# Kernel tuning notes

Hardware: AMD Instinct MI355X
Metric: run time of the kernel (lower is better)

## Reference

```python
import jax, jax.numpy as jnp
import numpy as np
from jax import lax

DN = ('NHWC', 'HWIO', 'NHWC')


def _conv(x, w):
    # x: [B,H,W,Cin], w: [kh,kw,Cin,Cout], 'same' padding
    return lax.conv_general_dilated(x, w, (1, 1), 'SAME', dimension_numbers=DN)


def _hard_sigmoid(x):
    # Keras hard_sigmoid: clip(0.2*x + 0.5, 0, 1)
    return jnp.clip(0.2 * x + 0.5, 0.0, 1.0)


def convlstm2d(x, Wk, Uk, b, filters):
    """Keras ConvLSTM2D, return_sequences=True, padding='same'.
    x: [B,T,H,W,Cin]. Gate order in kernel: [i, f, c, o].
    Returns h sequence [B,T,H,W,filters].
    """
    B, T, H, W, _ = x.shape
    h0 = jnp.zeros((B, H, W, filters), x.dtype)
    c0 = jnp.zeros((B, H, W, filters), x.dtype)

    def step(carry, xt):
        h, c = carry
        z = _conv(xt, Wk) + _conv(h, Uk) + b  # [B,H,W,4*filters]
        zi, zf, zc, zo = jnp.split(z, 4, axis=-1)
        i = _hard_sigmoid(zi)
        f = _hard_sigmoid(zf)
        o = _hard_sigmoid(zo)
        c_new = f * c + i * jnp.tanh(zc)
        h_new = o * jnp.tanh(c_new)
        return (h_new, c_new), h_new

    xs = jnp.moveaxis(x, 1, 0)  # [T,B,H,W,Cin]
    _, hs = lax.scan(step, (h0, c0), xs)
    return jnp.moveaxis(hs, 0, 1)  # [B,T,H,W,filters]


def setup_inputs() -> dict:
    key = jax.random.key(0)
    ks = jax.random.split(key, 7)
    B, T, H, W, Cin, F = 8, 10, 64, 64, 32, 64
    s = 0.05
    return {
        'x': jax.random.normal(ks[0], (B, T, H, W, Cin), jnp.float32),
        'Wk1': jax.random.normal(ks[1], (5, 5, Cin, 4 * F), jnp.float32) * s,
        'Uk1': jax.random.normal(ks[2], (5, 5, F, 4 * F), jnp.float32) * s,
        'b1': jnp.zeros((4 * F,), jnp.float32),
        'Wk2': jax.random.normal(ks[3], (3, 3, F, 4 * F), jnp.float32) * s,
        'Uk2': jax.random.normal(ks[4], (3, 3, F, 4 * F), jnp.float32) * s,
        'b2': jnp.zeros((4 * F,), jnp.float32),
    }


def reference(x, Wk1, Uk1, b1, Wk2, Uk2, b2):
    F = Uk1.shape[2]
    y = jax.nn.relu(convlstm2d(x, Wk1, Uk1, b1, F))
    y = jax.nn.relu(convlstm2d(y, Wk2, Uk2, b2, F))
    return y
```

## Files before the change

kernel.cpp:

```cpp
#include <hip/hip_runtime.h>
#include <cstdint>
#include <cmath>


#define NT 256

typedef __attribute__((ext_vector_type(8))) short short8;
typedef __attribute__((ext_vector_type(4))) float f32x4;

__device__ __forceinline__ float hsig(float v) {
    return fminf(fmaxf(fmaf(v, 0.2f, 0.5f), 0.0f), 1.0f);
}

__device__ __forceinline__ short bf16rnd(float f) {
    union { float f; unsigned u; } a; a.f = f;
    return (short)((a.u + 0x7FFFu + ((a.u >> 16) & 1u)) >> 16);
}

__device__ __forceinline__ void split_bf16(float f, short& h, short& l) {
    h = bf16rnd(f);
    union { unsigned u; float f; } b; b.u = ((unsigned)(unsigned short)h) << 16;
    l = bf16rnd(f - b.f);
}

__device__ __forceinline__ float from_bf16(short s) {
    union { unsigned u; float f; } b; b.u = ((unsigned)(unsigned short)s) << 16;
    return b.f;
}

template<int CIN, int KS>
__device__ __forceinline__ void conv_mfma(
    const short* __restrict__ P,
    const short* __restrict__ Bpk,
    f32x4 (&acc)[4][4],
    short* lds,
    int y, int fg, int lane, int tid)
{
    constexpr int PAD   = KS / 2;
    constexpr int COLS  = 64 + 2 * PAD;
    constexpr int PST   = 2 * CIN + 8;
    constexpr int CH    = CIN / 32;
    constexpr int VPP   = (2 * CIN) / 8;
    constexpr int NLOAD = COLS * VPP;
    constexpr int NV    = (NLOAD + NT - 1) / NT;

    uint4 vals[NV];

    auto load_row = [&](int ky) {
        int yin = y + ky - PAD;
        const short* rowp = P + (size_t)yin * 64 * 2 * CIN;
        #pragma unroll
        for (int i = 0; i < NV; ++i) {
            int idx = tid + i * NT;
            uint4 z; z.x = 0; z.y = 0; z.z = 0; z.w = 0;
            if (idx < NLOAD) {
                int col = idx / VPP;
                int v   = idx - col * VPP;
                int g   = col - PAD;
                if (yin >= 0 && yin < 64 && g >= 0 && g < 64)
                    z = *(const uint4*)(rowp + (size_t)g * 2 * CIN + v * 8);
            }
            vals[i] = z;
        }
    };

    load_row(0);
    for (int ky = 0; ky < KS; ++ky) {
        __syncthreads();
        #pragma unroll
        for (int i = 0; i < NV; ++i) {
            int idx = tid + i * NT;
            if (idx < NLOAD) {
                int col = idx / VPP;
                int v   = idx - col * VPP;
                *(uint4*)(lds + col * PST + v * 8) = vals[i];
            }
        }
        __syncthreads();
        if (ky + 1 < KS) load_row(ky + 1);

        int yin = y + ky - PAD;
        if (yin >= 0 && yin < 64) {
            for (int kx = 0; kx < KS; ++kx) {
                int tap = ky * KS + kx;
                #pragma unroll
                for (int ch = 0; ch < CH; ++ch) {
                    int choff = ch * 32 + ((lane >> 4) & 3) * 8;
                    short8 ah[4], al[4];
                    #pragma unroll
                    for (int mt = 0; mt < 4; ++mt) {
                        int col = mt * 16 + (lane & 15) + kx;
                        const short* base = lds + col * PST + choff;
                        ah[mt] = *(const short8*)base;
                        al[mt] = *(const short8*)(base + CIN);
                    }
                    const short* bp = Bpk
                        + ((size_t)((tap * CH + ch) * 16 + fg)) * 1024
                        + lane * 16;
                    #pragma unroll
                    for (int g = 0; g < 4; ++g) {
                        short8 bh = *(const short8*)bp;
                        short8 bl = *(const short8*)(bp + 8);
                        bp += 4096;
                        #pragma unroll
                        for (int mt = 0; mt < 4; ++mt) {
                            acc[g][mt] = __builtin_amdgcn_mfma_f32_16x16x32_bf16(
                                ah[mt], bh, acc[g][mt], 0, 0, 0);
                            acc[g][mt] = __builtin_amdgcn_mfma_f32_16x16x32_bf16(
                                al[mt], bh, acc[g][mt], 0, 0, 0);
                            acc[g][mt] = __builtin_amdgcn_mfma_f32_16x16x32_bf16(
                                ah[mt], bl, acc[g][mt], 0, 0, 0);
                        }
                    }
                }
            }
        }
    }
}

template<int CIN_X, int KS, bool WRITE_SEQ>
__global__ __launch_bounds__(NT, 2)
void convlstm_step(
    const short* __restrict__ xp, long xp_bstride,
    const short* __restrict__ h_prev,
    float* __restrict__ c_state,
    const short* __restrict__ Wpk,
    const short* __restrict__ Upk,
    const float* __restrict__ bias,
    short* __restrict__ h_next,
    short* __restrict__ seq, long seq_bstride)
{
    __shared__ __align__(16) short lds[9248];

    const int tid  = threadIdx.x;
    const int lane = tid & 63;
    const int fg   = tid >> 6;
    const int q    = (lane >> 4) & 3;
    const int batch = blockIdx.x >> 6;
    const int y     = blockIdx.x & 63;

    f32x4 acc[4][4];
    #pragma unroll
    for (int g = 0; g < 4; ++g)
        #pragma unroll
        for (int mt = 0; mt < 4; ++mt)
            #pragma unroll
            for (int r = 0; r < 4; ++r) acc[g][mt][r] = 0.0f;

    conv_mfma<CIN_X, KS>(xp + (size_t)batch * xp_bstride, Wpk, acc, lds, y, fg, lane, tid);
    conv_mfma<64,    KS>(h_prev + (size_t)batch * 4096 * 128, Upk, acc, lds, y, fg, lane, tid);

    const int fl = fg * 16 + (lane & 15);
    const float b_i = bias[fl];
    const float b_f = bias[64 + fl];
    const float b_c = bias[128 + fl];
    const float b_o = bias[192 + fl];

    const long pixbase = (long)batch * 4096 + (long)y * 64;
    const long cb = pixbase * 64 + fl;
    const long sb = (long)batch * seq_bstride + ((long)y * 64) * 128 + fl;

    #pragma unroll
    for (int mt = 0; mt < 4; ++mt) {
        #pragma unroll
        for (int r = 0; r < 4; ++r) {
            int col = mt * 16 + q * 4 + r;
            long cidx = cb + (long)col * 64;
            float zi = acc[0][mt][r] + b_i;
            float zf = acc[1][mt][r] + b_f;
            float zc = acc[2][mt][r] + b_c;
            float zo = acc[3][mt][r] + b_o;
            float ig = hsig(zi);
            float fgt = hsig(zf);
            float og = hsig(zo);
            float cp = c_state[cidx];
            float cn = fgt * cp + ig * tanhf(zc);
            float hn = og * tanhf(cn);
            c_state[cidx] = cn;

            short hh, hl;
            split_bf16(hn, hh, hl);
            long hoff = (pixbase + col) * 128 + fl;
            h_next[hoff]      = hh;
            h_next[hoff + 64] = hl;
            if (WRITE_SEQ) {
                bool pos = hn > 0.0f;
                seq[sb + (long)col * 128]      = pos ? hh : (short)0;
                seq[sb + (long)col * 128 + 64] = pos ? hl : (short)0;
            }
        }
    }
}

__global__ void convert_planes32(const float4* __restrict__ src,
                                 unsigned* __restrict__ dst, int n4)
{
    int t = blockIdx.x * NT + threadIdx.x;
    if (t >= n4) return;
    int pix = t >> 3;
    int c4  = t & 7;
    float4 v = src[t];
    short h0, l0, h1, l1, h2, l2, h3, l3;
    split_bf16(v.x, h0, l0);
    split_bf16(v.y, h1, l1);
    split_bf16(v.z, h2, l2);
    split_bf16(v.w, h3, l3);
    unsigned* p = dst + (size_t)pix * 32;
    p[c4 * 2]      = (unsigned)(unsigned short)h0 | ((unsigned)(unsigned short)h1 << 16);
    p[c4 * 2 + 1]  = (unsigned)(unsigned short)h2 | ((unsigned)(unsigned short)h3 << 16);
    p[16 + c4 * 2]     = (unsigned)(unsigned short)l0 | ((unsigned)(unsigned short)l1 << 16);
    p[16 + c4 * 2 + 1] = (unsigned)(unsigned short)l2 | ((unsigned)(unsigned short)l3 << 16);
}

__global__ void repack(const float* __restrict__ src, short* __restrict__ dst,
                       int KS, int CH)
{
    int total = KS * KS * CH * 16 * 64;
    int t = blockIdx.x * NT + threadIdx.x;
    if (t >= total) return;
    int u = t >> 6, lane = t & 63;
    int tap = u / (CH * 16);
    int rem = u - tap * (CH * 16);
    int ch = rem >> 4;
    int gfg = rem & 15;
    int g = gfg >> 2, fgp = gfg & 3;
    int CIN = CH * 32;
    int n = lane & 15, qq = lane >> 4;
    short* d = dst + (size_t)u * 1024 + lane * 16;
    int gc = g * 64 + fgp * 16 + n;
    for (int j = 0; j < 8; ++j) {
        int c = ch * 32 + qq * 8 + j;
        float w = src[((size_t)tap * CIN + c) * 256 + gc];
        short h, l;
        split_bf16(w, h, l);
        d[j] = h;
        d[8 + j] = l;
    }
}

__global__ void relu_copy(const short* __restrict__ hp, float* __restrict__ out,
                          long out_bstride)
{
    long i = (long)blockIdx.x * NT + threadIdx.x;
    long pix = i >> 6;
    int c = (int)(i & 63);
    float f = from_bf16(hp[pix * 128 + c]) + from_bf16(hp[pix * 128 + 64 + c]);
    long b = pix >> 12;
    long within = (pix & 4095) * 64 + c;
    out[b * out_bstride + within] = fmaxf(f, 0.0f);
}

extern "C" void kernel_launch(void* const* d_in, const int* in_sizes, int n_in,
                              void* d_out, int out_size, void* d_ws, size_t ws_size,
                              hipStream_t stream) {
    const float* x   = (const float*)d_in[0];
    const float* Wk1 = (const float*)d_in[1];
    const float* Uk1 = (const float*)d_in[2];
    const float* b1  = (const float*)d_in[3];
    const float* Wk2 = (const float*)d_in[4];
    const float* Uk2 = (const float*)d_in[5];
    const float* b2  = (const float*)d_in[6];
    float* out = (float*)d_out;

    const long S  = (long)8 * 64 * 64 * 64;
    const long oT = (long)64 * 64 * 64;
    const long oB = 10 * oT;

    short* h_a = (short*)d_ws;
    short* h_b = h_a + 2 * S;
    float* c_s = (float*)(h_b + 2 * S);
    short* Wp1 = (short*)(c_s + S);
    short* Up1 = Wp1 + 25 * 1 * 16 * 1024;
    short* Wp2 = Up1 + 25 * 2 * 16 * 1024;
    short* Up2 = Wp2 + 9 * 2 * 16 * 1024;
    short* x1p = Up2 + 9 * 2 * 16 * 1024;
    const long x1pN = (long)8 * 10 * 4096 * 64;
    (void)x1pN; (void)ws_size;

    {
        int n4 = 8 * 10 * 4096 * 8;
        convert_planes32<<<dim3((n4 + NT - 1) / NT), dim3(NT), 0, stream>>>(
            (const float4*)x, (unsigned*)x1p, n4);
    }
    repack<<<dim3((25 * 1 * 16 * 64 + NT - 1) / NT), dim3(NT), 0, stream>>>(Wk1, Wp1, 5, 1);
    repack<<<dim3((25 * 2 * 16 * 64 + NT - 1) / NT), dim3(NT), 0, stream>>>(Uk1, Up1, 5, 2);
    repack<<<dim3((9 * 2 * 16 * 64 + NT - 1) / NT), dim3(NT), 0, stream>>>(Wk2, Wp2, 3, 2);
    repack<<<dim3((9 * 2 * 16 * 64 + NT - 1) / NT), dim3(NT), 0, stream>>>(Uk2, Up2, 3, 2);

    short* seqs = (short*)d_out;

    hipMemsetAsync(h_a, 0, (size_t)S * 4, stream);
    hipMemsetAsync(c_s, 0, (size_t)S * 4, stream);
    short* hc = h_a;
    short* hn = h_b;
    const long x1T = (long)4096 * 64;
    const long x1B = 10 * x1T;
    for (int t = 0; t < 10; ++t) {
        convlstm_step<32, 5, true><<<dim3(512), dim3(NT), 0, stream>>>(
            x1p + t * x1T, x1B, hc, c_s, Wp1, Up1, b1, hn,
            seqs + t * oT * 2, oB * 2);
        short* tmp = hc; hc = hn; hn = tmp;
    }

    hipMemsetAsync(hc, 0, (size_t)S * 4, stream);
    hipMemsetAsync(c_s, 0, (size_t)S * 4, stream);
    for (int t = 0; t < 10; ++t) {
        convlstm_step<64, 3, false><<<dim3(512), dim3(NT), 0, stream>>>(
            seqs + t * oT * 2, oB * 2, hc, c_s, Wp2, Up2, b2, hn,
            nullptr, 0);
        relu_copy<<<dim3(8192), dim3(NT), 0, stream>>>(hn, out + t * oT, oB);
        short* tmp = hc; hc = hn; hn = tmp;
    }
}
```

Baseline: 1.946 ms.

## Split rows across two 2-wave blocks, fuse x/h convs, prefetch weights in registers

The step kernel now uses 128-thread blocks, each covering half of the filter groups for one output row, which doubles the grid to 1024 blocks. The x and h convolutions are merged into a single loop over kernel rows that stages both input rows in separate LDS buffers. Padding is handled by zero-filling LDS once and skipping out-of-range kernel rows. Weight fragments for the next tap/segment are software-prefetched into registers so global loads overlap the MFMAs. This costs more register pressure and duplicates the input-row loads across the two half-blocks.

```diff
diff --git a/kernel.cpp b/kernel.cpp
--- a/kernel.cpp
+++ b/kernel.cpp
@@ -3,7 +3,8 @@
 #include <cmath>
 
 
-#define NT 256
+#define NT  128
+#define NTU 256
 
 typedef __attribute__((ext_vector_type(8))) short short8;
 typedef __attribute__((ext_vector_type(4))) float f32x4;
@@ -28,97 +29,9 @@
     return b.f;
 }
 
-template<int CIN, int KS>
-__device__ __forceinline__ void conv_mfma(
-    const short* __restrict__ P,
-    const short* __restrict__ Bpk,
-    f32x4 (&acc)[4][4],
-    short* lds,
-    int y, int fg, int lane, int tid)
-{
-    constexpr int PAD   = KS / 2;
-    constexpr int COLS  = 64 + 2 * PAD;
-    constexpr int PST   = 2 * CIN + 8;
-    constexpr int CH    = CIN / 32;
-    constexpr int VPP   = (2 * CIN) / 8;
-    constexpr int NLOAD = COLS * VPP;
-    constexpr int NV    = (NLOAD + NT - 1) / NT;
-
-    uint4 vals[NV];
-
-    auto load_row = [&](int ky) {
-        int yin = y + ky - PAD;
-        const short* rowp = P + (size_t)yin * 64 * 2 * CIN;
-        #pragma unroll
-        for (int i = 0; i < NV; ++i) {
-            int idx = tid + i * NT;
-            uint4 z; z.x = 0; z.y = 0; z.z = 0; z.w = 0;
-            if (idx < NLOAD) {
-                int col = idx / VPP;
-                int v   = idx - col * VPP;
-                int g   = col - PAD;
-                if (yin >= 0 && yin < 64 && g >= 0 && g < 64)
-                    z = *(const uint4*)(rowp + (size_t)g * 2 * CIN + v * 8);
-            }
-            vals[i] = z;
-        }
-    };
-
-    load_row(0);
-    for (int ky = 0; ky < KS; ++ky) {
-        __syncthreads();
-        #pragma unroll
-        for (int i = 0; i < NV; ++i) {
-            int idx = tid + i * NT;
-            if (idx < NLOAD) {
-                int col = idx / VPP;
-                int v   = idx - col * VPP;
-                *(uint4*)(lds + col * PST + v * 8) = vals[i];
-            }
-        }
-        __syncthreads();
-        if (ky + 1 < KS) load_row(ky + 1);
-
-        int yin = y + ky - PAD;
-        if (yin >= 0 && yin < 64) {
-            for (int kx = 0; kx < KS; ++kx) {
-                int tap = ky * KS + kx;
-                #pragma unroll
-                for (int ch = 0; ch < CH; ++ch) {
-                    int choff = ch * 32 + ((lane >> 4) & 3) * 8;
-                    short8 ah[4], al[4];
-                    #pragma unroll
-                    for (int mt = 0; mt < 4; ++mt) {
-                        int col = mt * 16 + (lane & 15) + kx;
-                        const short* base = lds + col * PST + choff;
-                        ah[mt] = *(const short8*)base;
-                        al[mt] = *(const short8*)(base + CIN);
-                    }
-                    const short* bp = Bpk
-                        + ((size_t)((tap * CH + ch) * 16 + fg)) * 1024
-                        + lane * 16;
-                    #pragma unroll
-                    for (int g = 0; g < 4; ++g) {
-                        short8 bh = *(const short8*)bp;
-                        short8 bl = *(const short8*)(bp + 8);
-                        bp += 4096;
-                        #pragma unroll
-                        for (int mt = 0; mt < 4; ++mt) {
-                            acc[g][mt] = __builtin_amdgcn_mfma_f32_16x16x32_bf16(
-                                ah[mt], bh, acc[g][mt], 0, 0, 0);
-                            acc[g][mt] = __builtin_amdgcn_mfma_f32_16x16x32_bf16(
-                                al[mt], bh, acc[g][mt], 0, 0, 0);
-                            acc[g][mt] = __builtin_amdgcn_mfma_f32_16x16x32_bf16(
-                                ah[mt], bl, acc[g][mt], 0, 0, 0);
-                        }
-                    }
-                }
-            }
-        }
-    }
-}
-
-template<int CIN_X, int KS, bool WRITE_SEQ>
+struct BF { uint4 bh[4]; uint4 bl[4]; };
+
+template<int CINX, int KS, bool WRITE_SEQ>
 __global__ __launch_bounds__(NT, 2)
 void convlstm_step(
     const short* __restrict__ xp, long xp_bstride,
@@ -130,14 +43,39 @@
     short* __restrict__ h_next,
     short* __restrict__ seq, long seq_bstride)
 {
-    __shared__ __align__(16) short lds[9248];
+    constexpr int PAD  = KS / 2;
+    constexpr int COLS = 64 + 2 * PAD;
+    constexpr int CHX  = CINX / 32;
+    constexpr int SEGS = CHX + 2;
+    constexpr int PSTX = 2 * CINX + 8;
+    constexpr int PSTH = 136;
+    constexpr int VPPX = CINX / 4;
+
+    __shared__ __align__(16) short xs[COLS * PSTX];
+    __shared__ __align__(16) short hs[COLS * PSTH];
 
     const int tid  = threadIdx.x;
     const int lane = tid & 63;
-    const int fg   = tid >> 6;
-    const int q    = (lane >> 4) & 3;
-    const int batch = blockIdx.x >> 6;
-    const int y     = blockIdx.x & 63;
+    const int wid  = tid >> 6;
+    const int q8   = ((lane >> 4) & 3) * 8;
+    const int bi   = blockIdx.x;
+    const int batch = bi >> 7;
+    const int rem   = bi & 127;
+    const int y     = rem >> 1;
+    const int half  = rem & 1;
+    const int fg    = half * 2 + wid;
+
+    const short* xim = xp + (size_t)batch * xp_bstride;
+    const short* him = h_prev + (size_t)batch * 4096 * 128;
+
+    for (int idx = tid; idx < (COLS * PSTX) / 8; idx += NT) {
+        uint4 z; z.x = 0; z.y = 0; z.z = 0; z.w = 0;
+        *(uint4*)(xs + idx * 8) = z;
+    }
+    for (int idx = tid; idx < (COLS * PSTH) / 8; idx += NT) {
+        uint4 z; z.x = 0; z.y = 0; z.z = 0; z.w = 0;
+        *(uint4*)(hs + idx * 8) = z;
+    }
 
     f32x4 acc[4][4];
     #pragma unroll
@@ -147,14 +85,92 @@
             #pragma unroll
             for (int r = 0; r < 4; ++r) acc[g][mt][r] = 0.0f;
 
-    conv_mfma<CIN_X, KS>(xp + (size_t)batch * xp_bstride, Wpk, acc, lds, y, fg, lane, tid);
-    conv_mfma<64,    KS>(h_prev + (size_t)batch * 4096 * 128, Upk, acc, lds, y, fg, lane, tid);
+    auto loadB = [&](int ky, int kx, int s) -> BF {
+        int tap = ky * KS + kx;
+        const short* base;
+        if (s < CHX)
+            base = Wpk + ((size_t)((tap * CHX + s) * 16 + fg)) * 1024 + lane * 16;
+        else
+            base = Upk + ((size_t)((tap * 2 + (s - CHX)) * 16 + fg)) * 1024 + lane * 16;
+        BF b;
+        #pragma unroll
+        for (int g = 0; g < 4; ++g) {
+            b.bh[g] = *(const uint4*)(base + (size_t)g * 4096);
+            b.bl[g] = *(const uint4*)(base + (size_t)g * 4096 + 8);
+        }
+        return b;
+    };
+
+    const int ky0   = (y < PAD) ? (PAD - y) : 0;
+    const int kyend = (64 + PAD - y) < KS ? (64 + PAD - y) : KS;
+
+    BF bcur = loadB(ky0, 0, 0);
+
+    for (int ky = ky0; ky < kyend; ++ky) {
+        int yin = y + ky - PAD;
+        __syncthreads();
+        const short* xrow = xim + (size_t)yin * 64 * 2 * CINX;
+        for (int idx = tid; idx < 64 * VPPX; idx += NT) {
+            int px = idx / VPPX;
+            int v  = idx - px * VPPX;
+            *(uint4*)(xs + (px + PAD) * PSTX + v * 8)
+                = *(const uint4*)(xrow + px * 2 * CINX + v * 8);
+        }
+        const short* hrow = him + (size_t)yin * 64 * 128;
+        for (int idx = tid; idx < 64 * 16; idx += NT) {
+            int px = idx >> 4;
+            int v  = idx & 15;
+            *(uint4*)(hs + (px + PAD) * PSTH + v * 8)
+                = *(const uint4*)(hrow + px * 128 + v * 8);
+        }
+        __syncthreads();
+
+        #pragma unroll
+        for (int kx = 0; kx < KS; ++kx) {
+            #pragma unroll
+            for (int s = 0; s < SEGS; ++s) {
+                int ns = s + 1, nkx = kx, nky = ky;
+                if (ns == SEGS) { ns = 0; ++nkx; }
+                if (nkx == KS)  { nkx = 0; ++nky; }
+                if (nky >= kyend) { nky = ky; nkx = kx; ns = s; }
+                BF bnxt = loadB(nky, nkx, ns);
+
+                short8 ah[4], al[4];
+                #pragma unroll
+                for (int mt = 0; mt < 4; ++mt) {
+                    int col = mt * 16 + (lane & 15) + kx;
+                    const short* p = (s < CHX)
+                        ? (xs + col * PSTX + s * 32 + q8)
+                        : (hs + col * PSTH + (s - CHX) * 32 + q8);
+                    int lo = (s < CHX) ? CINX : 64;
+                    ah[mt] = *(const short8*)p;
+                    al[mt] = *(const short8*)(p + lo);
+                }
+                #pragma unroll
+                for (int g = 0; g < 4; ++g) {
+                    short8 bh = *(const short8*)&bcur.bh[g];
+                    short8 bl = *(const short8*)&bcur.bl[g];
+                    #pragma unroll
+                    for (int mt = 0; mt < 4; ++mt) {
+                        acc[g][mt] = __builtin_amdgcn_mfma_f32_16x16x32_bf16(
+                            ah[mt], bh, acc[g][mt], 0, 0, 0);
+                        acc[g][mt] = __builtin_amdgcn_mfma_f32_16x16x32_bf16(
+                            al[mt], bh, acc[g][mt], 0, 0, 0);
+                        acc[g][mt] = __builtin_amdgcn_mfma_f32_16x16x32_bf16(
+                            ah[mt], bl, acc[g][mt], 0, 0, 0);
+                    }
+                }
+                bcur = bnxt;
+            }
+        }
+    }
 
     const int fl = fg * 16 + (lane & 15);
     const float b_i = bias[fl];
     const float b_f = bias[64 + fl];
     const float b_c = bias[128 + fl];
     const float b_o = bias[192 + fl];
+    const int q = (lane >> 4) & 3;
 
     const long pixbase = (long)batch * 4096 + (long)y * 64;
     const long cb = pixbase * 64 + fl;
@@ -195,7 +211,7 @@
 __global__ void convert_planes32(const float4* __restrict__ src,
                                  unsigned* __restrict__ dst, int n4)
 {
-    int t = blockIdx.x * NT + threadIdx.x;
+    int t = blockIdx.x * NTU + threadIdx.x;
     if (t >= n4) return;
     int pix = t >> 3;
     int c4  = t & 7;
@@ -216,7 +232,7 @@
                        int KS, int CH)
 {
     int total = KS * KS * CH * 16 * 64;
-    int t = blockIdx.x * NT + threadIdx.x;
+    int t = blockIdx.x * NTU + threadIdx.x;
     if (t >= total) return;
     int u = t >> 6, lane = t & 63;
     int tap = u / (CH * 16);
@@ -241,7 +257,7 @@
 __global__ void relu_copy(const short* __restrict__ hp, float* __restrict__ out,
                           long out_bstride)
 {
-    long i = (long)blockIdx.x * NT + threadIdx.x;
+    long i = (long)blockIdx.x * NTU + threadIdx.x;
     long pix = i >> 6;
     int c = (int)(i & 63);
     float f = from_bf16(hp[pix * 128 + c]) + from_bf16(hp[pix * 128 + 64 + c]);
@@ -274,18 +290,17 @@
     short* Wp2 = Up1 + 25 * 2 * 16 * 1024;
     short* Up2 = Wp2 + 9 * 2 * 16 * 1024;
     short* x1p = Up2 + 9 * 2 * 16 * 1024;
-    const long x1pN = (long)8 * 10 * 4096 * 64;
-    (void)x1pN; (void)ws_size;
+    (void)ws_size;
 
     {
         int n4 = 8 * 10 * 4096 * 8;
-        convert_planes32<<<dim3((n4 + NT - 1) / NT), dim3(NT), 0, stream>>>(
+        convert_planes32<<<dim3((n4 + NTU - 1) / NTU), dim3(NTU), 0, stream>>>(
             (const float4*)x, (unsigned*)x1p, n4);
     }
-    repack<<<dim3((25 * 1 * 16 * 64 + NT - 1) / NT), dim3(NT), 0, stream>>>(Wk1, Wp1, 5, 1);
-    repack<<<dim3((25 * 2 * 16 * 64 + NT - 1) / NT), dim3(NT), 0, stream>>>(Uk1, Up1, 5, 2);
-    repack<<<dim3((9 * 2 * 16 * 64 + NT - 1) / NT), dim3(NT), 0, stream>>>(Wk2, Wp2, 3, 2);
-    repack<<<dim3((9 * 2 * 16 * 64 + NT - 1) / NT), dim3(NT), 0, stream>>>(Uk2, Up2, 3, 2);
+    repack<<<dim3((25 * 1 * 16 * 64 + NTU - 1) / NTU), dim3(NTU), 0, stream>>>(Wk1, Wp1, 5, 1);
+    repack<<<dim3((25 * 2 * 16 * 64 + NTU - 1) / NTU), dim3(NTU), 0, stream>>>(Uk1, Up1, 5, 2);
+    repack<<<dim3((9 * 2 * 16 * 64 + NTU - 1) / NTU), dim3(NTU), 0, stream>>>(Wk2, Wp2, 3, 2);
+    repack<<<dim3((9 * 2 * 16 * 64 + NTU - 1) / NTU), dim3(NTU), 0, stream>>>(Uk2, Up2, 3, 2);
 
     short* seqs = (short*)d_out;
 
@@ -296,7 +311,7 @@
     const long x1T = (long)4096 * 64;
     const long x1B = 10 * x1T;
     for (int t = 0; t < 10; ++t) {
-        convlstm_step<32, 5, true><<<dim3(512), dim3(NT), 0, stream>>>(
+        convlstm_step<32, 5, true><<<dim3(1024), dim3(NT), 0, stream>>>(
             x1p + t * x1T, x1B, hc, c_s, Wp1, Up1, b1, hn,
             seqs + t * oT * 2, oB * 2);
         short* tmp = hc; hc = hn; hn = tmp;
@@ -305,10 +320,10 @@
     hipMemsetAsync(hc, 0, (size_t)S * 4, stream);
     hipMemsetAsync(c_s, 0, (size_t)S * 4, stream);
     for (int t = 0; t < 10; ++t) {
-        convlstm_step<64, 3, false><<<dim3(512), dim3(NT), 0, stream>>>(
+        convlstm_step<64, 3, false><<<dim3(1024), dim3(NT), 0, stream>>>(
             seqs + t * oT * 2, oB * 2, hc, c_s, Wp2, Up2, b2, hn,
             nullptr, 0);
-        relu_copy<<<dim3(8192), dim3(NT), 0, stream>>>(hn, out + t * oT, oB);
+        relu_copy<<<dim3(8192), dim3(NTU), 0, stream>>>(hn, out + t * oT, oB);
         short* tmp = hc; hc = hn; hn = tmp;
     }
 }
```

Result: slower. 2.062 ms (+5.9%).
